# Kernel tuning notes

Measured on AMD Instinct MI355X. Metric: run time of the kernel, lower is better.

## Reference

```python
import jax, jax.numpy as jnp
import numpy as np

N = 50000  # num nodes


def _gcn_layer(x, W, b, src, dst, dinv):
    # PyG GCNConv: transform first, then normalized neighbor aggregation
    h = x @ W                                   # [N, out]
    norm = dinv[src] * dinv[dst]                # [E]
    msg = h[src] * norm[:, None]                # gather + scale, [E, out]
    agg = jax.ops.segment_sum(msg, dst, num_segments=N)
    agg = agg + h * (dinv * dinv)[:, None]      # self-loop term (weight 1)
    return agg + b


def setup_inputs() -> dict:
    key = jax.random.key(0)
    ks = jax.random.split(key, 9)
    x = jax.random.normal(ks[0], (N, 256), dtype=jnp.float32)
    edge_index = jax.random.randint(ks[1], (2, 800000), 0, N, dtype=jnp.int64)
    def lin(kw, kb, fan_in, fan_out):
        s = 1.0 / np.sqrt(fan_in)
        W = jax.random.uniform(kw, (fan_in, fan_out), jnp.float32, -s, s)
        b = jax.random.uniform(kb, (fan_out,), jnp.float32, -s, s)
        return W, b
    W0, b0 = lin(ks[2], ks[3], 256, 128)
    W1, b1 = lin(ks[4], ks[5], 128, 128)
    W2, b2 = lin(ks[6], ks[7], 128, 64)
    return {"x": x, "edge_index": edge_index,
            "W0": W0, "b0": b0, "W1": W1, "b1": b1, "W2": W2, "b2": b2}


def reference(x, edge_index, W0, b0, W1, b1, W2, b2):
    src, dst = edge_index[0], edge_index[1]
    # degree with implicit self loops (edge weights = 1)
    deg = jax.ops.segment_sum(jnp.ones_like(dst, dtype=x.dtype), dst,
                              num_segments=N) + 1.0
    dinv = jax.lax.rsqrt(deg)
    h = jax.nn.relu(_gcn_layer(x, W0, b0, src, dst, dinv))
    h = jax.nn.relu(_gcn_layer(h, W1, b1, src, dst, dinv))
    out = _gcn_layer(h, W2, b2, src, dst, dinv)  # no relu on final layer
    return out
```

## Files before the change

### kernel.cpp

```cpp
#include <hip/hip_runtime.h>

#define NNODES 50000
#define NEDGES 800000
#define CHUNK 3125

typedef __attribute__((ext_vector_type(8))) short short8;
typedef __attribute__((ext_vector_type(4))) float floatx4;
typedef __attribute__((ext_vector_type(8))) _Float16 f16x8;

__device__ __forceinline__ void async16(const void* g, void* l) {
    __builtin_amdgcn_global_load_lds(
        (const __attribute__((address_space(1))) unsigned int*)g,
        (__attribute__((address_space(3))) unsigned int*)l, 16, 0, 0);
}

__device__ __forceinline__ void split_bf16(float v, short& hi, short& lo) {
    unsigned u = __float_as_uint(v);
    unsigned hu = u & 0xffff0000u;
    hi = (short)(hu >> 16);
    float r = v - __uint_as_float(hu);
    lo = (short)(__float_as_uint(r) >> 16);
}


#define PREP_WBLK 224
#define PREP_TOT  (PREP_WBLK + 256)

__global__ __launch_bounds__(256) void k_prep(
    const float* __restrict__ W0, short* __restrict__ W0h, short* __restrict__ W0l,
    const float* __restrict__ W1, short* __restrict__ W1h, short* __restrict__ W1l,
    const float* __restrict__ W2, short* __restrict__ W2h, short* __restrict__ W2l,
    const int* __restrict__ dst, int* __restrict__ hist2d) {
    int b = blockIdx.x, t = threadIdx.x;
    if (b < PREP_WBLK) {
        int id = b * 256 + t;
        const float* W; short *Wh, *Wl; int K, F;
        if (id < 32768) { W = W0; Wh = W0h; Wl = W0l; K = 256; F = 128; }
        else if (id < 49152) { id -= 32768; W = W1; Wh = W1h; Wl = W1l; K = 128; F = 128; }
        else if (id < 57344) { id -= 49152; W = W2; Wh = W2h; Wl = W2l; K = 128; F = 64; }
        else return;
        int f = id / K, k = id - f * K;
        short h, l;
        split_bf16(W[(size_t)k * F + f], h, l);
        Wh[id] = h;
        Wl[id] = l;
    } else {
        __shared__ int h[256];
        int bb = b - PREP_WBLK;
        h[t] = 0;
        __syncthreads();
        int e0 = bb * CHUNK;
#pragma unroll
        for (int k = 0; k < 13; k++) {
            int o = k * 256 + t;
            if (o < CHUNK) atomicAdd(&h[dst[e0 + o] >> 8], 1);
        }
        __syncthreads();
        hist2d[bb * 256 + t] = h[t];
    }
}

__global__ __launch_bounds__(256) void k_p2(const int* __restrict__ src,
                                            const int* __restrict__ dst,
                                            const int* __restrict__ hist2d,
                                            unsigned* __restrict__ buck) {
    __shared__ int ex[256], cur[256];
    int t = threadIdx.x, b = blockIdx.x;
    int tot = 0, pre = 0;
    for (int bb = 0; bb < 256; bb++) {
        int v = hist2d[bb * 256 + t];
        tot += v;
        pre += (bb < b) ? v : 0;
    }
    ex[t] = tot;
    __syncthreads();
    for (int o = 1; o < 256; o <<= 1) {
        int xx = (t >= o) ? ex[t - o] : 0;
        __syncthreads();
        ex[t] += xx;
        __syncthreads();
    }
    cur[t] = (ex[t] - tot) + pre;
    __syncthreads();
    int e0 = b * CHUNK;
#pragma unroll
    for (int k = 0; k < 13; k++) {
        int o = k * 256 + t;
        if (o < CHUNK) {
            int s = src[e0 + o], d = dst[e0 + o];
            int p = atomicAdd(&cur[d >> 8], 1);
            buck[p] = (unsigned)s | ((unsigned)(d & 255) << 16);
        }
    }
}

__global__ __launch_bounds__(256) void k_p3(const unsigned* __restrict__ buck,
                                            const int* __restrict__ hist2d,
                                            int* __restrict__ rowptr,
                                            float* __restrict__ dinv,
                                            int* __restrict__ ssrc) {
    __shared__ int ex[256], cur[256], h[256], sS0[1], sS[1];
    int t = threadIdx.x, b = blockIdx.x;
    int tot = 0;
    for (int bb = 0; bb < 256; bb++) tot += hist2d[bb * 256 + t];
    ex[t] = tot;
    __syncthreads();
    for (int o = 1; o < 256; o <<= 1) {
        int xx = (t >= o) ? ex[t - o] : 0;
        __syncthreads();
        ex[t] += xx;
        __syncthreads();
    }
    if (t == b) { sS0[0] = ex[t] - tot; sS[0] = tot; }
    h[t] = 0;
    __syncthreads();
    int s0 = sS0[0], S = sS[0];
    for (int i = t; i < S; i += 256)
        atomicAdd(&h[(buck[s0 + i] >> 16) & 255], 1);
    __syncthreads();
    int v = h[t];
    ex[t] = v;
    __syncthreads();
    for (int o = 1; o < 256; o <<= 1) {
        int xx = (t >= o) ? ex[t - o] : 0;
        __syncthreads();
        ex[t] += xx;
        __syncthreads();
    }
    int excl = ex[t] - v;
    int n = b * 256 + t;
    if (n < NNODES) {
        rowptr[n] = s0 + excl;
        dinv[n] = rsqrtf((float)v + 1.0f);
    }
    if (b == 0 && t == 0) rowptr[NNODES] = NEDGES;
    cur[t] = excl;
    __syncthreads();
    for (int i = t; i < S; i += 256) {
        unsigned pk = buck[s0 + i];
        int dl = (pk >> 16) & 255;
        int p = atomicAdd(&cur[dl], 1);
        ssrc[s0 + p] = (int)(pk & 0xFFFFu);
    }
}


__global__ __launch_bounds__(256) void k_gemm0(
    const float* __restrict__ x, const short* __restrict__ Bh,
    const short* __restrict__ Bl, const float* __restrict__ dinv,
    _Float16* __restrict__ g16) {
    __shared__ __align__(16) short sAh[64 * 64], sAl[64 * 64];
    __shared__ __align__(16) short sBh[128 * 64], sBl[128 * 64];
    const int t = threadIdx.x, lane = t & 63, w = t >> 6;
    const int row0 = blockIdx.x * 64;
    const int lr = lane >> 3, lz = lane & 7;
    const int swz = (lz ^ lr) * 8;
    const int fr = lane & 15, fq = lane >> 4;
    floatx4 acc[8] = {};
    const int ar = t >> 2, ac = t & 3;
    int garow = row0 + ar;
    if (garow >= NNODES) garow = NNODES - 1;
    const float* xrow = x + (size_t)garow * 256 + ac * 16;

    for (int k0 = 0; k0 < 256; k0 += 64) {
        const float4* xp = (const float4*)(xrow + k0);
        float4 f0 = xp[0], f1 = xp[1], f2 = xp[2], f3 = xp[3];
        float va[16] = {f0.x, f0.y, f0.z, f0.w, f1.x, f1.y, f1.z, f1.w,
                        f2.x, f2.y, f2.z, f2.w, f3.x, f3.y, f3.z, f3.w};
        short8 h0, h1, l0, l1;
#pragma unroll
        for (int j = 0; j < 8; j++) {
            short h, l;
            split_bf16(va[j], h, l);     h0[j] = h; l0[j] = l;
            split_bf16(va[8 + j], h, l); h1[j] = h; l1[j] = l;
        }
        int c0 = ac * 2;
        *(short8*)&sAh[ar * 64 + ((c0 ^ (ar & 7)) * 8)] = h0;
        *(short8*)&sAh[ar * 64 + (((c0 + 1) ^ (ar & 7)) * 8)] = h1;
        *(short8*)&sAl[ar * 64 + ((c0 ^ (ar & 7)) * 8)] = l0;
        *(short8*)&sAl[ar * 64 + (((c0 + 1) ^ (ar & 7)) * 8)] = l1;
#pragma unroll
        for (int jj = 0; jj < 4; jj++) {
            int j = w * 4 + jj;
            size_t go = (size_t)(j * 8 + lr) * 256 + k0 + swz;
            async16(&Bh[go], &sBh[j * 512 + lane * 8]);
            async16(&Bl[go], &sBl[j * 512 + lane * 8]);
        }
        __syncthreads();
#pragma unroll
        for (int ks = 0; ks < 2; ks++) {
            int R = w * 16 + fr;
            int ca = ((ks * 4 + fq) ^ (R & 7)) * 8;
            short8 ah = *(const short8*)&sAh[R * 64 + ca];
            short8 al = *(const short8*)&sAl[R * 64 + ca];
#pragma unroll
            for (int nt = 0; nt < 8; nt++) {
                int n = nt * 16 + fr;
                int cb = ((ks * 4 + fq) ^ (n & 7)) * 8;
                short8 bh = *(const short8*)&sBh[n * 64 + cb];
                short8 bl = *(const short8*)&sBl[n * 64 + cb];
                acc[nt] = __builtin_amdgcn_mfma_f32_16x16x32_bf16(ah, bh, acc[nt], 0, 0, 0);
                acc[nt] = __builtin_amdgcn_mfma_f32_16x16x32_bf16(ah, bl, acc[nt], 0, 0, 0);
                acc[nt] = __builtin_amdgcn_mfma_f32_16x16x32_bf16(al, bh, acc[nt], 0, 0, 0);
            }
        }
        __syncthreads();
    }
#pragma unroll
    for (int rr = 0; rr < 4; rr++) {
        int grow = row0 + w * 16 + fq * 4 + rr;
        if (grow < NNODES) {
            float dv = dinv[grow];
#pragma unroll
            for (int nt = 0; nt < 8; nt++)
                g16[(size_t)grow * 128 + nt * 16 + fr] =
                    (_Float16)(acc[nt][rr] * dv);
        }
    }
}


template <int BN>
__global__ __launch_bounds__(256) void k_fg(
    const _Float16* __restrict__ gin, const int* __restrict__ ssrc,
    const int* __restrict__ rowptr, const float* __restrict__ dinv,
    const float* __restrict__ bias, const short* __restrict__ Bh,
    const short* __restrict__ Bl, _Float16* __restrict__ gout) {
    constexpr int NT = BN / 16;
    __shared__ __align__(16) short sAh[64 * 128], sAl[64 * 128];
    __shared__ __align__(16) short sBh[BN * 32], sBl[BN * 32];
    const int t = threadIdx.x, lane = t & 63, w = t >> 6;
    const int row0 = blockIdx.x * 64;
    const int fr = lane & 15, fq = lane >> 4;
    const f16x8* gp = (const f16x8*)gin;

    const int cc = t & 15;
#pragma unroll
    for (int pass = 0; pass < 4; pass++) {
        int r = pass * 16 + (t >> 4);
        int grow = row0 + r;
        if (grow >= NNODES) grow = NNODES - 1;
        f16x8 sv = gp[(size_t)grow * 16 + cc];
        float a0[8], a1[8], a2[8], a3[8];
#pragma unroll
        for (int j = 0; j < 8; j++) {
            a0[j] = (float)sv[j];
            a1[j] = 0.f; a2[j] = 0.f; a3[j] = 0.f;
        }
        int e0 = rowptr[grow], e1 = rowptr[grow + 1];
        int e = e0;
        for (; e + 4 <= e1; e += 4) {
            int s0 = ssrc[e], s1 = ssrc[e + 1], s2 = ssrc[e + 2], s3 = ssrc[e + 3];
            f16x8 v0 = gp[(size_t)s0 * 16 + cc];
            f16x8 v1 = gp[(size_t)s1 * 16 + cc];
            f16x8 v2 = gp[(size_t)s2 * 16 + cc];
            f16x8 v3 = gp[(size_t)s3 * 16 + cc];
#pragma unroll
            for (int j = 0; j < 8; j++) {
                a0[j] += (float)v0[j];
                a1[j] += (float)v1[j];
                a2[j] += (float)v2[j];
                a3[j] += (float)v3[j];
            }
        }
        for (; e < e1; e++) {
            int s = ssrc[e];
            f16x8 v = gp[(size_t)s * 16 + cc];
#pragma unroll
            for (int j = 0; j < 8; j++) a0[j] += (float)v[j];
        }
        float dv = dinv[grow];
        short8 h8, l8;
#pragma unroll
        for (int j = 0; j < 8; j++) {
            float s = (a0[j] + a1[j]) + (a2[j] + a3[j]);
            float o = fmaxf(s * dv + bias[cc * 8 + j], 0.f);
            short hh, ll;
            split_bf16(o, hh, ll);
            h8[j] = hh; l8[j] = ll;
        }
        int slot = ((cc & 7) ^ (r & 7)) + (cc >> 3) * 8;
        *(short8*)&sAh[r * 128 + slot * 8] = h8;
        *(short8*)&sAl[r * 128 + slot * 8] = l8;
    }
    __syncthreads();

    floatx4 acc[NT] = {};
    const int lrB = lane >> 2, lzB = lane & 3;
    for (int q = 0; q < 4; q++) {
#pragma unroll
        for (int jj = 0; jj < BN / 64; jj++) {
            int j = w * (BN / 64) + jj;
            int brow = j * 16 + lrB;
            size_t go = (size_t)brow * 128 + q * 32 + ((lzB ^ (lrB & 3)) * 8);
            async16(&Bh[go], &sBh[j * 512 + lane * 8]);
            async16(&Bl[go], &sBl[j * 512 + lane * 8]);
        }
        __syncthreads();
        int R = w * 16 + fr;
        int c = q * 4 + fq;
        int slotA = ((c & 7) ^ (R & 7)) + (c >> 3) * 8;
        short8 ah = *(const short8*)&sAh[R * 128 + slotA * 8];
        short8 al = *(const short8*)&sAl[R * 128 + slotA * 8];
#pragma unroll
        for (int nt = 0; nt < NT; nt++) {
            int n = nt * 16 + fr;
            short8 bh = *(const short8*)&sBh[n * 32 + ((fq ^ (n & 3)) * 8)];
            short8 bl = *(const short8*)&sBl[n * 32 + ((fq ^ (n & 3)) * 8)];
            acc[nt] = __builtin_amdgcn_mfma_f32_16x16x32_bf16(ah, bh, acc[nt], 0, 0, 0);
            acc[nt] = __builtin_amdgcn_mfma_f32_16x16x32_bf16(ah, bl, acc[nt], 0, 0, 0);
            acc[nt] = __builtin_amdgcn_mfma_f32_16x16x32_bf16(al, bh, acc[nt], 0, 0, 0);
        }
        __syncthreads();
    }

#pragma unroll
    for (int rr = 0; rr < 4; rr++) {
        int grow = row0 + w * 16 + fq * 4 + rr;
        if (grow < NNODES) {
            float dv = dinv[grow];
#pragma unroll
            for (int nt = 0; nt < NT; nt++)
                gout[(size_t)grow * BN + nt * 16 + fr] =
                    (_Float16)(acc[nt][rr] * dv);
        }
    }
}


template <int F>
__global__ __launch_bounds__(256) void k_agg(const _Float16* __restrict__ g,
                                             const int* __restrict__ ssrc,
                                             const int* __restrict__ rowptr,
                                             const float* __restrict__ dinv,
                                             const float* __restrict__ bias,
                                             float* __restrict__ outf) {
    constexpr int F8 = F / 8;
    int gid = blockIdx.x * 256 + threadIdx.x;
    int n = gid / F8;
    if (n >= NNODES) return;
    int c8 = gid - n * F8;
    const f16x8* gp = (const f16x8*)g;

    f16x8 sv = gp[(size_t)n * F8 + c8];
    float a0[8], a1[8], a2[8], a3[8];
#pragma unroll
    for (int j = 0; j < 8; j++) {
        a0[j] = (float)sv[j];
        a1[j] = 0.f; a2[j] = 0.f; a3[j] = 0.f;
    }
    int e0 = rowptr[n], e1 = rowptr[n + 1];
    int e = e0;
    for (; e + 4 <= e1; e += 4) {
        int s0 = ssrc[e], s1 = ssrc[e + 1], s2 = ssrc[e + 2], s3 = ssrc[e + 3];
        f16x8 v0 = gp[(size_t)s0 * F8 + c8];
        f16x8 v1 = gp[(size_t)s1 * F8 + c8];
        f16x8 v2 = gp[(size_t)s2 * F8 + c8];
        f16x8 v3 = gp[(size_t)s3 * F8 + c8];
#pragma unroll
        for (int j = 0; j < 8; j++) {
            a0[j] += (float)v0[j];
            a1[j] += (float)v1[j];
            a2[j] += (float)v2[j];
            a3[j] += (float)v3[j];
        }
    }
    for (; e < e1; e++) {
        int s = ssrc[e];
        f16x8 v = gp[(size_t)s * F8 + c8];
#pragma unroll
        for (int j = 0; j < 8; j++) a0[j] += (float)v[j];
    }
    float dv = dinv[n];
    float o[8];
#pragma unroll
    for (int j = 0; j < 8; j++) {
        float s = (a0[j] + a1[j]) + (a2[j] + a3[j]);
        o[j] = s * dv + bias[c8 * 8 + j];
    }
    *(float4*)&outf[(size_t)n * F + c8 * 8] = make_float4(o[0], o[1], o[2], o[3]);
    *(float4*)&outf[(size_t)n * F + c8 * 8 + 4] = make_float4(o[4], o[5], o[6], o[7]);
}


static inline size_t align256(size_t x) { return (x + 255) & ~(size_t)255; }

extern "C" void kernel_launch(void* const* d_in, const int* in_sizes, int n_in,
                              void* d_out, int out_size, void* d_ws, size_t ws_size,
                              hipStream_t stream) {
    const float* x  = (const float*)d_in[0];
    const int*   ei = (const int*)d_in[1];
    const float* W0 = (const float*)d_in[2];
    const float* b0 = (const float*)d_in[3];
    const float* W1 = (const float*)d_in[4];
    const float* b1 = (const float*)d_in[5];
    const float* W2 = (const float*)d_in[6];
    const float* b2 = (const float*)d_in[7];
    float* out = (float*)d_out;

    const int* src = ei;
    const int* dst = ei + NEDGES;

    char* w = (char*)d_ws;
    size_t off = 0;
    float* dinv    = (float*)(w + off); off = align256(off + NNODES * 4);
    int* rowptr    = (int*)(w + off);   off = align256(off + (NNODES + 1) * 4);
    int* hist2d    = (int*)(w + off);   off = align256(off + 256 * 256 * 4);
    unsigned* buck = (unsigned*)(w + off); off = align256(off + (size_t)NEDGES * 4);
    int* ssrc      = (int*)(w + off);   off = align256(off + (size_t)NEDGES * 4);
    short* W0h     = (short*)(w + off); off = align256(off + 256 * 128 * 2);
    short* W0l     = (short*)(w + off); off = align256(off + 256 * 128 * 2);
    short* W1h     = (short*)(w + off); off = align256(off + 128 * 128 * 2);
    short* W1l     = (short*)(w + off); off = align256(off + 128 * 128 * 2);
    short* W2h     = (short*)(w + off); off = align256(off + 128 * 64 * 2);
    short* W2l     = (short*)(w + off); off = align256(off + 128 * 64 * 2);
    _Float16* g16a = (_Float16*)(w + off); off = align256(off + (size_t)NNODES * 128 * 2);
    _Float16* g16b = (_Float16*)(w + off); off = align256(off + (size_t)NNODES * 128 * 2);
    _Float16* g16c = (_Float16*)(w + off); off = align256(off + (size_t)NNODES * 64 * 2);

    const int MB = (NNODES + 63) / 64;
    const int AB64 = (NNODES * 8 + 255) / 256;

    k_prep<<<PREP_TOT, 256, 0, stream>>>(W0, W0h, W0l, W1, W1h, W1l,
                                         W2, W2h, W2l, dst, hist2d);
    k_p2<<<256, 256, 0, stream>>>(src, dst, hist2d, buck);
    k_p3<<<256, 256, 0, stream>>>(buck, hist2d, rowptr, dinv, ssrc);
    k_gemm0<<<MB, 256, 0, stream>>>(x, W0h, W0l, dinv, g16a);
    k_fg<128><<<MB, 256, 0, stream>>>(g16a, ssrc, rowptr, dinv, b0, W1h, W1l, g16b);
    k_fg<64><<<MB, 256, 0, stream>>>(g16b, ssrc, rowptr, dinv, b1, W2h, W2l, g16c);
    k_agg<64><<<AB64, 256, 0, stream>>>(g16c, ssrc, rowptr, dinv, b2, out);
    (void)in_sizes; (void)n_in; (void)out_size; (void)ws_size;
}
```

Baseline: 267.9 us.

## Load A operands directly into MFMA registers, dropping shared-memory A staging

```diff
diff --git a/kernel.cpp b/kernel.cpp
--- a/kernel.cpp
+++ b/kernel.cpp
@@ -145,75 +145,71 @@
 }
 
 
+template <int BN, int K>
+__device__ __forceinline__ void stage_b(const short* __restrict__ Bh,
+                                        const short* __restrict__ Bl,
+                                        short* sBh, short* sBl,
+                                        int w, int lane, int q) {
+    constexpr int JJN = BN / 64;
+#pragma unroll
+    for (int jj = 0; jj < JJN; jj++) {
+        int j = w * JJN + jj;
+        int l = j * 64 + lane;
+        int c = l / BN, n = l % BN;
+        size_t go = (size_t)n * K + q * 32 + c * 8;
+        async16(&Bh[go], &sBh[l * 8]);
+        async16(&Bl[go], &sBl[l * 8]);
+    }
+}
+
+
 __global__ __launch_bounds__(256) void k_gemm0(
     const float* __restrict__ x, const short* __restrict__ Bh,
     const short* __restrict__ Bl, const float* __restrict__ dinv,
     _Float16* __restrict__ g16) {
-    __shared__ __align__(16) short sAh[64 * 64], sAl[64 * 64];
-    __shared__ __align__(16) short sBh[128 * 64], sBl[128 * 64];
+    __shared__ __align__(16) short sBh[512 * 8], sBl[512 * 8];
     const int t = threadIdx.x, lane = t & 63, w = t >> 6;
     const int row0 = blockIdx.x * 64;
-    const int lr = lane >> 3, lz = lane & 7;
-    const int swz = (lz ^ lr) * 8;
     const int fr = lane & 15, fq = lane >> 4;
+    int grow = row0 + w * 16 + fr;
+    if (grow >= NNODES) grow = NNODES - 1;
+    const float* xr = x + (size_t)grow * 256 + fq * 8;
+
     floatx4 acc[8] = {};
-    const int ar = t >> 2, ac = t & 3;
-    int garow = row0 + ar;
-    if (garow >= NNODES) garow = NNODES - 1;
-    const float* xrow = x + (size_t)garow * 256 + ac * 16;
-
-    for (int k0 = 0; k0 < 256; k0 += 64) {
-        const float4* xp = (const float4*)(xrow + k0);
-        float4 f0 = xp[0], f1 = xp[1], f2 = xp[2], f3 = xp[3];
-        float va[16] = {f0.x, f0.y, f0.z, f0.w, f1.x, f1.y, f1.z, f1.w,
-                        f2.x, f2.y, f2.z, f2.w, f3.x, f3.y, f3.z, f3.w};
-        short8 h0, h1, l0, l1;
+    stage_b<128, 256>(Bh, Bl, sBh, sBl, w, lane, 0);
+
+    for (int q = 0; q < 8; q++) {
+        const float4* xp = (const float4*)(xr + q * 32);
+        float4 f0 = xp[0], f1 = xp[1];
+        float va[8] = {f0.x, f0.y, f0.z, f0.w, f1.x, f1.y, f1.z, f1.w};
+        short8 ah, al;
 #pragma unroll
         for (int j = 0; j < 8; j++) {
             short h, l;
-            split_bf16(va[j], h, l);     h0[j] = h; l0[j] = l;
-            split_bf16(va[8 + j], h, l); h1[j] = h; l1[j] = l;
-        }
-        int c0 = ac * 2;
-        *(short8*)&sAh[ar * 64 + ((c0 ^ (ar & 7)) * 8)] = h0;
-        *(short8*)&sAh[ar * 64 + (((c0 + 1) ^ (ar & 7)) * 8)] = h1;
-        *(short8*)&sAl[ar * 64 + ((c0 ^ (ar & 7)) * 8)] = l0;
-        *(short8*)&sAl[ar * 64 + (((c0 + 1) ^ (ar & 7)) * 8)] = l1;
-#pragma unroll
-        for (int jj = 0; jj < 4; jj++) {
-            int j = w * 4 + jj;
-            size_t go = (size_t)(j * 8 + lr) * 256 + k0 + swz;
-            async16(&Bh[go], &sBh[j * 512 + lane * 8]);
-            async16(&Bl[go], &sBl[j * 512 + lane * 8]);
-        }
-        __syncthreads();
-#pragma unroll
-        for (int ks = 0; ks < 2; ks++) {
-            int R = w * 16 + fr;
-            int ca = ((ks * 4 + fq) ^ (R & 7)) * 8;
-            short8 ah = *(const short8*)&sAh[R * 64 + ca];
-            short8 al = *(const short8*)&sAl[R * 64 + ca];
-#pragma unroll
-            for (int nt = 0; nt < 8; nt++) {
-                int n = nt * 16 + fr;
-                int cb = ((ks * 4 + fq) ^ (n & 7)) * 8;
-                short8 bh = *(const short8*)&sBh[n * 64 + cb];
-                short8 bl = *(const short8*)&sBl[n * 64 + cb];
-                acc[nt] = __builtin_amdgcn_mfma_f32_16x16x32_bf16(ah, bh, acc[nt], 0, 0, 0);
-                acc[nt] = __builtin_amdgcn_mfma_f32_16x16x32_bf16(ah, bl, acc[nt], 0, 0, 0);
-                acc[nt] = __builtin_amdgcn_mfma_f32_16x16x32_bf16(al, bh, acc[nt], 0, 0, 0);
-            }
+            split_bf16(va[j], h, l);
+            ah[j] = h; al[j] = l;
+        }
+        if (q > 0) stage_b<128, 256>(Bh, Bl, sBh, sBl, w, lane, q);
+        __syncthreads();
+#pragma unroll
+        for (int nt = 0; nt < 8; nt++) {
+            int sl = fq * 128 + nt * 16 + fr;
+            short8 bh = *(const short8*)&sBh[sl * 8];
+            short8 bl = *(const short8*)&sBl[sl * 8];
+            acc[nt] = __builtin_amdgcn_mfma_f32_16x16x32_bf16(ah, bh, acc[nt], 0, 0, 0);
+            acc[nt] = __builtin_amdgcn_mfma_f32_16x16x32_bf16(ah, bl, acc[nt], 0, 0, 0);
+            acc[nt] = __builtin_amdgcn_mfma_f32_16x16x32_bf16(al, bh, acc[nt], 0, 0, 0);
         }
         __syncthreads();
     }
 #pragma unroll
     for (int rr = 0; rr < 4; rr++) {
-        int grow = row0 + w * 16 + fq * 4 + rr;
-        if (grow < NNODES) {
-            float dv = dinv[grow];
+        int gw = row0 + w * 16 + fq * 4 + rr;
+        if (gw < NNODES) {
+            float dv = dinv[gw];
 #pragma unroll
             for (int nt = 0; nt < 8; nt++)
-                g16[(size_t)grow * 128 + nt * 16 + fr] =
+                g16[(size_t)gw * 128 + nt * 16 + fr] =
                     (_Float16)(acc[nt][rr] * dv);
         }
     }
@@ -227,102 +223,86 @@
     const float* __restrict__ bias, const short* __restrict__ Bh,
     const short* __restrict__ Bl, _Float16* __restrict__ gout) {
     constexpr int NT = BN / 16;
-    __shared__ __align__(16) short sAh[64 * 128], sAl[64 * 128];
-    __shared__ __align__(16) short sBh[BN * 32], sBl[BN * 32];
+    __shared__ __align__(16) short sBh[4 * BN * 8], sBl[4 * BN * 8];
     const int t = threadIdx.x, lane = t & 63, w = t >> 6;
     const int row0 = blockIdx.x * 64;
     const int fr = lane & 15, fq = lane >> 4;
     const f16x8* gp = (const f16x8*)gin;
 
-    const int cc = t & 15;
-#pragma unroll
-    for (int pass = 0; pass < 4; pass++) {
-        int r = pass * 16 + (t >> 4);
-        int grow = row0 + r;
-        if (grow >= NNODES) grow = NNODES - 1;
-        f16x8 sv = gp[(size_t)grow * 16 + cc];
-        float a0[8], a1[8], a2[8], a3[8];
+    stage_b<BN, 128>(Bh, Bl, sBh, sBl, w, lane, 0);
+
+    int grow = row0 + w * 16 + fr;
+    if (grow >= NNODES) grow = NNODES - 1;
+    float acc[4][8];
+#pragma unroll
+    for (int q = 0; q < 4; q++) {
+        f16x8 sv = gp[(size_t)grow * 16 + q * 4 + fq];
+#pragma unroll
+        for (int j = 0; j < 8; j++) acc[q][j] = (float)sv[j];
+    }
+    int e0 = rowptr[grow], e1 = rowptr[grow + 1];
+    int e = e0;
+    for (; e + 2 <= e1; e += 2) {
+        int s0 = ssrc[e], s1 = ssrc[e + 1];
+        f16x8 u[4], v[4];
+#pragma unroll
+        for (int q = 0; q < 4; q++) {
+            u[q] = gp[(size_t)s0 * 16 + q * 4 + fq];
+            v[q] = gp[(size_t)s1 * 16 + q * 4 + fq];
+        }
+#pragma unroll
+        for (int q = 0; q < 4; q++)
+#pragma unroll
+            for (int j = 0; j < 8; j++)
+                acc[q][j] += (float)u[q][j] + (float)v[q][j];
+    }
+    for (; e < e1; e++) {
+        int s = ssrc[e];
+#pragma unroll
+        for (int q = 0; q < 4; q++) {
+            f16x8 u = gp[(size_t)s * 16 + q * 4 + fq];
+#pragma unroll
+            for (int j = 0; j < 8; j++) acc[q][j] += (float)u[j];
+        }
+    }
+    float dv = dinv[grow];
+    short8 ah[4], al[4];
+#pragma unroll
+    for (int q = 0; q < 4; q++) {
 #pragma unroll
         for (int j = 0; j < 8; j++) {
-            a0[j] = (float)sv[j];
-            a1[j] = 0.f; a2[j] = 0.f; a3[j] = 0.f;
-        }
-        int e0 = rowptr[grow], e1 = rowptr[grow + 1];
-        int e = e0;
-        for (; e + 4 <= e1; e += 4) {
-            int s0 = ssrc[e], s1 = ssrc[e + 1], s2 = ssrc[e + 2], s3 = ssrc[e + 3];
-            f16x8 v0 = gp[(size_t)s0 * 16 + cc];
-            f16x8 v1 = gp[(size_t)s1 * 16 + cc];
-            f16x8 v2 = gp[(size_t)s2 * 16 + cc];
-            f16x8 v3 = gp[(size_t)s3 * 16 + cc];
-#pragma unroll
-            for (int j = 0; j < 8; j++) {
-                a0[j] += (float)v0[j];
-                a1[j] += (float)v1[j];
-                a2[j] += (float)v2[j];
-                a3[j] += (float)v3[j];
-            }
-        }
-        for (; e < e1; e++) {
-            int s = ssrc[e];
-            f16x8 v = gp[(size_t)s * 16 + cc];
-#pragma unroll
-            for (int j = 0; j < 8; j++) a0[j] += (float)v[j];
-        }
-        float dv = dinv[grow];
-        short8 h8, l8;
-#pragma unroll
-        for (int j = 0; j < 8; j++) {
-            float s = (a0[j] + a1[j]) + (a2[j] + a3[j]);
-            float o = fmaxf(s * dv + bias[cc * 8 + j], 0.f);
+            float o = fmaxf(acc[q][j] * dv + bias[(q * 4 + fq) * 8 + j], 0.f);
             short hh, ll;
             split_bf16(o, hh, ll);
-            h8[j] = hh; l8[j] = ll;
-        }
-        int slot = ((cc & 7) ^ (r & 7)) + (cc >> 3) * 8;
-        *(short8*)&sAh[r * 128 + slot * 8] = h8;
-        *(short8*)&sAl[r * 128 + slot * 8] = l8;
-    }
-    __syncthreads();
-
-    floatx4 acc[NT] = {};
-    const int lrB = lane >> 2, lzB = lane & 3;
+            ah[q][j] = hh; al[q][j] = ll;
+        }
+    }
+
+    floatx4 accC[NT] = {};
     for (int q = 0; q < 4; q++) {
-#pragma unroll
-        for (int jj = 0; jj < BN / 64; jj++) {
-            int j = w * (BN / 64) + jj;
-            int brow = j * 16 + lrB;
-            size_t go = (size_t)brow * 128 + q * 32 + ((lzB ^ (lrB & 3)) * 8);
-            async16(&Bh[go], &sBh[j * 512 + lane * 8]);
-            async16(&Bl[go], &sBl[j * 512 + lane * 8]);
-        }
-        __syncthreads();
-        int R = w * 16 + fr;
-        int c = q * 4 + fq;
-        int slotA = ((c & 7) ^ (R & 7)) + (c >> 3) * 8;
-        short8 ah = *(const short8*)&sAh[R * 128 + slotA * 8];
-        short8 al = *(const short8*)&sAl[R * 128 + slotA * 8];
+        if (q > 0) stage_b<BN, 128>(Bh, Bl, sBh, sBl, w, lane, q);
+        __syncthreads();
 #pragma unroll
         for (int nt = 0; nt < NT; nt++) {
-            int n = nt * 16 + fr;
-            short8 bh = *(const short8*)&sBh[n * 32 + ((fq ^ (n & 3)) * 8)];
-            short8 bl = *(const short8*)&sBl[n * 32 + ((fq ^ (n & 3)) * 8)];
-            acc[nt] = __builtin_amdgcn_mfma_f32_16x16x32_bf16(ah, bh, acc[nt], 0, 0, 0);
-            acc[nt] = __builtin_amdgcn_mfma_f32_16x16x32_bf16(ah, bl, acc[nt], 0, 0, 0);
-            acc[nt] = __builtin_amdgcn_mfma_f32_16x16x32_bf16(al, bh, acc[nt], 0, 0, 0);
+            int sl = fq * BN + nt * 16 + fr;
+            short8 bh = *(const short8*)&sBh[sl * 8];
+            short8 bl = *(const short8*)&sBl[sl * 8];
+            accC[nt] = __builtin_amdgcn_mfma_f32_16x16x32_bf16(ah[q], bh, accC[nt], 0, 0, 0);
+            accC[nt] = __builtin_amdgcn_mfma_f32_16x16x32_bf16(ah[q], bl, accC[nt], 0, 0, 0);
+            accC[nt] = __builtin_amdgcn_mfma_f32_16x16x32_bf16(al[q], bh, accC[nt], 0, 0, 0);
         }
         __syncthreads();
     }
 
 #pragma unroll
     for (int rr = 0; rr < 4; rr++) {
-        int grow = row0 + w * 16 + fq * 4 + rr;
-        if (grow < NNODES) {
-            float dv = dinv[grow];
+        int gw = row0 + w * 16 + fq * 4 + rr;
+        if (gw < NNODES) {
+            float dv2 = dinv[gw];
 #pragma unroll
             for (int nt = 0; nt < NT; nt++)
-                gout[(size_t)grow * BN + nt * 16 + fr] =
-                    (_Float16)(acc[nt][rr] * dv);
+                gout[(size_t)gw * BN + nt * 16 + fr] =
+                    (_Float16)(accC[nt][rr] * dv2);
         }
     }
 }
```

New measurement: 299.7 us. 11.9% more time.

## Use column-chunked feature layout for gathers and unfuse aggregation from GEMM

Applied to the files above, without the earlier changes.

```diff
diff --git a/kernel.cpp b/kernel.cpp
--- a/kernel.cpp
+++ b/kernel.cpp
@@ -145,10 +145,17 @@
 }
 
 
+__device__ __forceinline__ void store_t(_Float16* gt, int nt, int fr, int grow,
+                                        float val) {
+    int c = nt * 2 + (fr >> 3);
+    gt[((size_t)c * NNODES + grow) * 8 + (fr & 7)] = (_Float16)val;
+}
+
+
 __global__ __launch_bounds__(256) void k_gemm0(
     const float* __restrict__ x, const short* __restrict__ Bh,
     const short* __restrict__ Bl, const float* __restrict__ dinv,
-    _Float16* __restrict__ g16) {
+    _Float16* __restrict__ gt) {
     __shared__ __align__(16) short sAh[64 * 64], sAl[64 * 64];
     __shared__ __align__(16) short sBh[128 * 64], sBl[128 * 64];
     const int t = threadIdx.x, lane = t & 63, w = t >> 6;
@@ -208,108 +215,71 @@
     }
 #pragma unroll
     for (int rr = 0; rr < 4; rr++) {
-        int grow = row0 + w * 16 + fq * 4 + rr;
-        if (grow < NNODES) {
-            float dv = dinv[grow];
+        int gw = row0 + w * 16 + fq * 4 + rr;
+        if (gw < NNODES) {
+            float dv = dinv[gw];
 #pragma unroll
             for (int nt = 0; nt < 8; nt++)
-                g16[(size_t)grow * 128 + nt * 16 + fr] =
-                    (_Float16)(acc[nt][rr] * dv);
+                store_t(gt, nt, fr, gw, acc[nt][rr] * dv);
         }
     }
 }
 
 
 template <int BN>
-__global__ __launch_bounds__(256) void k_fg(
-    const _Float16* __restrict__ gin, const int* __restrict__ ssrc,
-    const int* __restrict__ rowptr, const float* __restrict__ dinv,
-    const float* __restrict__ bias, const short* __restrict__ Bh,
-    const short* __restrict__ Bl, _Float16* __restrict__ gout) {
+__global__ __launch_bounds__(256) void k_gemm2(
+    const short* __restrict__ Ah, const short* __restrict__ Al,
+    const short* __restrict__ Bh, const short* __restrict__ Bl,
+    const float* __restrict__ dinv, _Float16* __restrict__ gt, int K) {
+    constexpr int BM = 64, BK = 64;
     constexpr int NT = BN / 16;
-    __shared__ __align__(16) short sAh[64 * 128], sAl[64 * 128];
-    __shared__ __align__(16) short sBh[BN * 32], sBl[BN * 32];
-    const int t = threadIdx.x, lane = t & 63, w = t >> 6;
-    const int row0 = blockIdx.x * 64;
+    __shared__ __align__(16) short sAh[BM * BK], sAl[BM * BK];
+    __shared__ __align__(16) short sBh[BN * BK], sBl[BN * BK];
+
+    const int tid = threadIdx.x, lane = tid & 63, w = tid >> 6;
+    const int row0 = blockIdx.x * BM;
+    const int lr = lane >> 3;
+    const int lz = lane & 7;
+    const int swz = (lz ^ lr) * 8;
     const int fr = lane & 15, fq = lane >> 4;
-    const f16x8* gp = (const f16x8*)gin;
-
-    const int cc = t & 15;
-#pragma unroll
-    for (int pass = 0; pass < 4; pass++) {
-        int r = pass * 16 + (t >> 4);
-        int grow = row0 + r;
-        if (grow >= NNODES) grow = NNODES - 1;
-        f16x8 sv = gp[(size_t)grow * 16 + cc];
-        float a0[8], a1[8], a2[8], a3[8];
-#pragma unroll
-        for (int j = 0; j < 8; j++) {
-            a0[j] = (float)sv[j];
-            a1[j] = 0.f; a2[j] = 0.f; a3[j] = 0.f;
-        }
-        int e0 = rowptr[grow], e1 = rowptr[grow + 1];
-        int e = e0;
-        for (; e + 4 <= e1; e += 4) {
-            int s0 = ssrc[e], s1 = ssrc[e + 1], s2 = ssrc[e + 2], s3 = ssrc[e + 3];
-            f16x8 v0 = gp[(size_t)s0 * 16 + cc];
-            f16x8 v1 = gp[(size_t)s1 * 16 + cc];
-            f16x8 v2 = gp[(size_t)s2 * 16 + cc];
-            f16x8 v3 = gp[(size_t)s3 * 16 + cc];
-#pragma unroll
-            for (int j = 0; j < 8; j++) {
-                a0[j] += (float)v0[j];
-                a1[j] += (float)v1[j];
-                a2[j] += (float)v2[j];
-                a3[j] += (float)v3[j];
+
+    floatx4 acc[NT] = {};
+
+    for (int k0 = 0; k0 < K; k0 += BK) {
+#pragma unroll
+        for (int jj = 0; jj < 2; jj++) {
+            int j = w * 2 + jj;
+            int grow = row0 + j * 8 + lr;
+            if (grow >= NNODES) grow = NNODES - 1;
+            size_t go = (size_t)grow * K + k0 + swz;
+            async16(&Ah[go], &sAh[j * 8 * BK + lane * 8]);
+            async16(&Al[go], &sAl[j * 8 * BK + lane * 8]);
+        }
+#pragma unroll
+        for (int jj = 0; jj < BN / 32; jj++) {
+            int j = w * (BN / 32) + jj;
+            size_t go = (size_t)(j * 8 + lr) * K + k0 + swz;
+            async16(&Bh[go], &sBh[j * 8 * BK + lane * 8]);
+            async16(&Bl[go], &sBl[j * 8 * BK + lane * 8]);
+        }
+        __syncthreads();
+
+#pragma unroll
+        for (int ks = 0; ks < 2; ks++) {
+            int R = w * 16 + fr;
+            int ca = ((ks * 4 + fq) ^ (R & 7)) * 8;
+            short8 ah = *(const short8*)&sAh[R * BK + ca];
+            short8 al = *(const short8*)&sAl[R * BK + ca];
+#pragma unroll
+            for (int nt = 0; nt < NT; nt++) {
+                int n = nt * 16 + fr;
+                int cb = ((ks * 4 + fq) ^ (n & 7)) * 8;
+                short8 bh = *(const short8*)&sBh[n * BK + cb];
+                short8 bl = *(const short8*)&sBl[n * BK + cb];
+                acc[nt] = __builtin_amdgcn_mfma_f32_16x16x32_bf16(ah, bh, acc[nt], 0, 0, 0);
+                acc[nt] = __builtin_amdgcn_mfma_f32_16x16x32_bf16(ah, bl, acc[nt], 0, 0, 0);
+                acc[nt] = __builtin_amdgcn_mfma_f32_16x16x32_bf16(al, bh, acc[nt], 0, 0, 0);
             }
-        }
-        for (; e < e1; e++) {
-            int s = ssrc[e];
-            f16x8 v = gp[(size_t)s * 16 + cc];
-#pragma unroll
-            for (int j = 0; j < 8; j++) a0[j] += (float)v[j];
-        }
-        float dv = dinv[grow];
-        short8 h8, l8;
-#pragma unroll
-        for (int j = 0; j < 8; j++) {
-            float s = (a0[j] + a1[j]) + (a2[j] + a3[j]);
-            float o = fmaxf(s * dv + bias[cc * 8 + j], 0.f);
-            short hh, ll;
-            split_bf16(o, hh, ll);
-            h8[j] = hh; l8[j] = ll;
-        }
-        int slot = ((cc & 7) ^ (r & 7)) + (cc >> 3) * 8;
-        *(short8*)&sAh[r * 128 + slot * 8] = h8;
-        *(short8*)&sAl[r * 128 + slot * 8] = l8;
-    }
-    __syncthreads();
-
-    floatx4 acc[NT] = {};
-    const int lrB = lane >> 2, lzB = lane & 3;
-    for (int q = 0; q < 4; q++) {
-#pragma unroll
-        for (int jj = 0; jj < BN / 64; jj++) {
-            int j = w * (BN / 64) + jj;
-            int brow = j * 16 + lrB;
-            size_t go = (size_t)brow * 128 + q * 32 + ((lzB ^ (lrB & 3)) * 8);
-            async16(&Bh[go], &sBh[j * 512 + lane * 8]);
-            async16(&Bl[go], &sBl[j * 512 + lane * 8]);
-        }
-        __syncthreads();
-        int R = w * 16 + fr;
-        int c = q * 4 + fq;
-        int slotA = ((c & 7) ^ (R & 7)) + (c >> 3) * 8;
-        short8 ah = *(const short8*)&sAh[R * 128 + slotA * 8];
-        short8 al = *(const short8*)&sAl[R * 128 + slotA * 8];
-#pragma unroll
-        for (int nt = 0; nt < NT; nt++) {
-            int n = nt * 16 + fr;
-            short8 bh = *(const short8*)&sBh[n * 32 + ((fq ^ (n & 3)) * 8)];
-            short8 bl = *(const short8*)&sBl[n * 32 + ((fq ^ (n & 3)) * 8)];
-            acc[nt] = __builtin_amdgcn_mfma_f32_16x16x32_bf16(ah, bh, acc[nt], 0, 0, 0);
-            acc[nt] = __builtin_amdgcn_mfma_f32_16x16x32_bf16(ah, bl, acc[nt], 0, 0, 0);
-            acc[nt] = __builtin_amdgcn_mfma_f32_16x16x32_bf16(al, bh, acc[nt], 0, 0, 0);
         }
         __syncthreads();
     }
@@ -321,28 +291,24 @@
             float dv = dinv[grow];
 #pragma unroll
             for (int nt = 0; nt < NT; nt++)
-                gout[(size_t)grow * BN + nt * 16 + fr] =
-                    (_Float16)(acc[nt][rr] * dv);
-        }
-    }
-}
-
-
-template <int F>
-__global__ __launch_bounds__(256) void k_agg(const _Float16* __restrict__ g,
-                                             const int* __restrict__ ssrc,
-                                             const int* __restrict__ rowptr,
-                                             const float* __restrict__ dinv,
-                                             const float* __restrict__ bias,
-                                             float* __restrict__ outf) {
-    constexpr int F8 = F / 8;
-    int gid = blockIdx.x * 256 + threadIdx.x;
-    int n = gid / F8;
+                store_t(gt, nt, fr, grow, acc[nt][rr] * dv);
+        }
+    }
+}
+
+
+__global__ __launch_bounds__(256) void k_aggt128(
+    const _Float16* __restrict__ gt, const int* __restrict__ ssrc,
+    const int* __restrict__ rowptr, const float* __restrict__ dinv,
+    const float* __restrict__ bias, short* __restrict__ oh,
+    short* __restrict__ ol) {
+    int b = blockIdx.x, t = threadIdx.x;
+    int c = (b & 7) + 8 * (t & 1);
+    int n = (b >> 3) * 128 + (t >> 1);
     if (n >= NNODES) return;
-    int c8 = gid - n * F8;
-    const f16x8* gp = (const f16x8*)g;
-
-    f16x8 sv = gp[(size_t)n * F8 + c8];
+    const f16x8* gp = (const f16x8*)gt + (size_t)c * NNODES;
+
+    f16x8 sv = gp[n];
     float a0[8], a1[8], a2[8], a3[8];
 #pragma unroll
     for (int j = 0; j < 8; j++) {
@@ -353,10 +319,7 @@
     int e = e0;
     for (; e + 4 <= e1; e += 4) {
         int s0 = ssrc[e], s1 = ssrc[e + 1], s2 = ssrc[e + 2], s3 = ssrc[e + 3];
-        f16x8 v0 = gp[(size_t)s0 * F8 + c8];
-        f16x8 v1 = gp[(size_t)s1 * F8 + c8];
-        f16x8 v2 = gp[(size_t)s2 * F8 + c8];
-        f16x8 v3 = gp[(size_t)s3 * F8 + c8];
+        f16x8 v0 = gp[s0], v1 = gp[s1], v2 = gp[s2], v3 = gp[s3];
 #pragma unroll
         for (int j = 0; j < 8; j++) {
             a0[j] += (float)v0[j];
@@ -366,8 +329,56 @@
         }
     }
     for (; e < e1; e++) {
-        int s = ssrc[e];
-        f16x8 v = gp[(size_t)s * F8 + c8];
+        f16x8 v = gp[ssrc[e]];
+#pragma unroll
+        for (int j = 0; j < 8; j++) a0[j] += (float)v[j];
+    }
+    float dv = dinv[n];
+    short8 h8, l8;
+#pragma unroll
+    for (int j = 0; j < 8; j++) {
+        float s = (a0[j] + a1[j]) + (a2[j] + a3[j]);
+        float o = fmaxf(s * dv + bias[c * 8 + j], 0.f);
+        short hh, ll;
+        split_bf16(o, hh, ll);
+        h8[j] = hh; l8[j] = ll;
+    }
+    *(short8*)&oh[(size_t)n * 128 + c * 8] = h8;
+    *(short8*)&ol[(size_t)n * 128 + c * 8] = l8;
+}
+
+__global__ __launch_bounds__(256) void k_aggt64(
+    const _Float16* __restrict__ gt, const int* __restrict__ ssrc,
+    const int* __restrict__ rowptr, const float* __restrict__ dinv,
+    const float* __restrict__ bias, float* __restrict__ outf) {
+    int b = blockIdx.x, t = threadIdx.x;
+    int c = b & 7;
+    int n = (b >> 3) * 256 + t;
+    if (n >= NNODES) return;
+    const f16x8* gp = (const f16x8*)gt + (size_t)c * NNODES;
+
+    f16x8 sv = gp[n];
+    float a0[8], a1[8], a2[8], a3[8];
+#pragma unroll
+    for (int j = 0; j < 8; j++) {
+        a0[j] = (float)sv[j];
+        a1[j] = 0.f; a2[j] = 0.f; a3[j] = 0.f;
+    }
+    int e0 = rowptr[n], e1 = rowptr[n + 1];
+    int e = e0;
+    for (; e + 4 <= e1; e += 4) {
+        int s0 = ssrc[e], s1 = ssrc[e + 1], s2 = ssrc[e + 2], s3 = ssrc[e + 3];
+        f16x8 v0 = gp[s0], v1 = gp[s1], v2 = gp[s2], v3 = gp[s3];
+#pragma unroll
+        for (int j = 0; j < 8; j++) {
+            a0[j] += (float)v0[j];
+            a1[j] += (float)v1[j];
+            a2[j] += (float)v2[j];
+            a3[j] += (float)v3[j];
+        }
+    }
+    for (; e < e1; e++) {
+        f16x8 v = gp[ssrc[e]];
 #pragma unroll
         for (int j = 0; j < 8; j++) a0[j] += (float)v[j];
     }
@@ -376,10 +387,10 @@
 #pragma unroll
     for (int j = 0; j < 8; j++) {
         float s = (a0[j] + a1[j]) + (a2[j] + a3[j]);
-        o[j] = s * dv + bias[c8 * 8 + j];
-    }
-    *(float4*)&outf[(size_t)n * F + c8 * 8] = make_float4(o[0], o[1], o[2], o[3]);
-    *(float4*)&outf[(size_t)n * F + c8 * 8 + 4] = make_float4(o[4], o[5], o[6], o[7]);
+        o[j] = s * dv + bias[c * 8 + j];
+    }
+    *(float4*)&outf[(size_t)n * 64 + c * 8] = make_float4(o[0], o[1], o[2], o[3]);
+    *(float4*)&outf[(size_t)n * 64 + c * 8 + 4] = make_float4(o[4], o[5], o[6], o[7]);
 }
 
 
@@ -414,20 +425,25 @@
     short* W1l     = (short*)(w + off); off = align256(off + 128 * 128 * 2);
     short* W2h     = (short*)(w + off); off = align256(off + 128 * 64 * 2);
     short* W2l     = (short*)(w + off); off = align256(off + 128 * 64 * 2);
-    _Float16* g16a = (_Float16*)(w + off); off = align256(off + (size_t)NNODES * 128 * 2);
-    _Float16* g16b = (_Float16*)(w + off); off = align256(off + (size_t)NNODES * 128 * 2);
-    _Float16* g16c = (_Float16*)(w + off); off = align256(off + (size_t)NNODES * 64 * 2);
+    short* ph      = (short*)(w + off); off = align256(off + (size_t)NNODES * 128 * 2);
+    short* pl      = (short*)(w + off); off = align256(off + (size_t)NNODES * 128 * 2);
+    _Float16* gt0  = (_Float16*)(w + off); off = align256(off + (size_t)NNODES * 128 * 2);
+    _Float16* gt1  = (_Float16*)(w + off); off = align256(off + (size_t)NNODES * 128 * 2);
+    _Float16* gt2  = (_Float16*)(w + off); off = align256(off + (size_t)NNODES * 64 * 2);
 
     const int MB = (NNODES + 63) / 64;
-    const int AB64 = (NNODES * 8 + 255) / 256;
+    const int AT128 = 8 * ((NNODES + 127) / 128);
+    const int AT64  = 8 * ((NNODES + 255) / 256);
 
     k_prep<<<PREP_TOT, 256, 0, stream>>>(W0, W0h, W0l, W1, W1h, W1l,
                                          W2, W2h, W2l, dst, hist2d);
     k_p2<<<256, 256, 0, stream>>>(src, dst, hist2d, buck);
     k_p3<<<256, 256, 0, stream>>>(buck, hist2d, rowptr, dinv, ssrc);
-    k_gemm0<<<MB, 256, 0, stream>>>(x, W0h, W0l, dinv, g16a);
-    k_fg<128><<<MB, 256, 0, stream>>>(g16a, ssrc, rowptr, dinv, b0, W1h, W1l, g16b);
-    k_fg<64><<<MB, 256, 0, stream>>>(g16b, ssrc, rowptr, dinv, b1, W2h, W2l, g16c);
-    k_agg<64><<<AB64, 256, 0, stream>>>(g16c, ssrc, rowptr, dinv, b2, out);
+    k_gemm0<<<MB, 256, 0, stream>>>(x, W0h, W0l, dinv, gt0);
+    k_aggt128<<<AT128, 256, 0, stream>>>(gt0, ssrc, rowptr, dinv, b0, ph, pl);
+    k_gemm2<128><<<MB, 256, 0, stream>>>(ph, pl, W1h, W1l, dinv, gt1, 128);
+    k_aggt128<<<AT128, 256, 0, stream>>>(gt1, ssrc, rowptr, dinv, b1, ph, pl);
+    k_gemm2<64><<<MB, 256, 0, stream>>>(ph, pl, W2h, W2l, dinv, gt2, 128);
+    k_aggt64<<<AT64, 256, 0, stream>>>(gt2, ssrc, rowptr, dinv, b2, out);
     (void)in_sizes; (void)n_in; (void)out_size; (void)ws_size;
 }
```

Result: slower. 366.5 us (+36.8%).
